# Kernel tuning notes

Measured on AMD Instinct MI355X. Metric: run time of the kernel, lower is better.

Reference implementation:

```python
import jax, jax.numpy as jnp
import numpy as np

N = 20000   # nodes
E = 40000   # directed edges
F_IN = 13   # dataset.num_features
G = 1000    # graphs in batch
DIMS = [(13, 32), (32, 64), (64, 64)]  # (M_in, M_out) per NNConv layer


def setup_inputs() -> dict:
    key = jax.random.key(0)
    ks = list(jax.random.split(key, 32))
    inp = {}
    inp["x"] = jax.random.normal(ks[0], (N, F_IN), jnp.float32)
    inp["edge_index"] = jax.random.randint(ks[1], (2, E), 0, N, dtype=jnp.int32)
    inp["edge_attr"] = jax.random.uniform(ks[2], (E, 5), dtype=jnp.float32)
    inp["batch"] = jnp.sort(jax.random.randint(ks[3], (N,), 0, G, dtype=jnp.int32))
    i = 4
    for l, (mi, mo) in enumerate(DIMS):
        inp[f"w1_{l}"] = jax.random.normal(ks[i], (5, 128), jnp.float32) / np.sqrt(5.0).astype(np.float32); i += 1
        inp[f"b1_{l}"] = jnp.zeros((128,), jnp.float32)
        inp[f"w2_{l}"] = jax.random.normal(ks[i], (128, mi * mo), jnp.float32) / np.sqrt(128.0).astype(np.float32); i += 1
        inp[f"b2_{l}"] = jnp.zeros((mi * mo,), jnp.float32)
        inp[f"root_{l}"] = jax.random.normal(ks[i], (mi, mo), jnp.float32) / np.sqrt(float(mi)).astype(np.float32); i += 1
        inp[f"bias_{l}"] = jnp.zeros((mo,), jnp.float32)
    inp["fc1_w"] = jax.random.normal(ks[i], (64, 32), jnp.float32) / 8.0; i += 1
    inp["fc1_b"] = jnp.zeros((32,), jnp.float32)
    inp["fc2_w"] = jax.random.normal(ks[i], (32, 16), jnp.float32) / np.sqrt(32.0).astype(np.float32); i += 1
    inp["fc2_b"] = jnp.zeros((16,), jnp.float32)
    inp["fc3_w"] = jax.random.normal(ks[i], (16, 1), jnp.float32) / 4.0; i += 1
    inp["fc3_b"] = jnp.zeros((1,), jnp.float32)
    return inp


def _nnconv(x, src, dst, edge_attr, w1, b1, w2, b2, root, bias, mi, mo):
    # edge MLP: [E,5] -> [E,128] -> [E, mi*mo] per-edge weight matrices
    h = jax.nn.relu(edge_attr @ w1 + b1)
    We = (h @ w2 + b2).reshape(-1, mi, mo)          # [E, mi, mo]
    msg = jnp.einsum('ei,eio->eo', x[src], We)      # gather + per-edge matmul
    agg = jax.ops.segment_sum(msg, dst, num_segments=x.shape[0])  # scatter-add
    return x @ root + agg + bias                    # NNConv root weight + bias


def _forward(x, edge_index, edge_attr, batch, convs, fc1_w, fc1_b, fc2_w, fc2_b, fc3_w, fc3_b):
    src, dst = edge_index[0], edge_index[1]
    for (mi, mo), (w1, b1, w2, b2, root, bias) in zip(DIMS, convs):
        x = jax.nn.elu(_nnconv(x, src, dst, edge_attr, w1, b1, w2, b2, root, bias, mi, mo))
    # scatter_mean pooling over graphs
    sums = jax.ops.segment_sum(x, batch, num_segments=G)
    cnt = jax.ops.segment_sum(jnp.ones((x.shape[0],), x.dtype), batch, num_segments=G)
    xg = sums / jnp.maximum(cnt, 1.0)[:, None]
    xg = jax.nn.elu(xg @ fc1_w + fc1_b)
    xg = jax.nn.elu(xg @ fc2_w + fc2_b)
    return (xg @ fc3_w + fc3_b).reshape(-1)


def reference(x, edge_index, edge_attr, batch,
              w1_0, b1_0, w2_0, b2_0, root_0, bias_0,
              w1_1, b1_1, w2_1, b2_1, root_1, bias_1,
              w1_2, b1_2, w2_2, b2_2, root_2, bias_2,
              fc1_w, fc1_b, fc2_w, fc2_b, fc3_w, fc3_b):
    convs = [(w1_0, b1_0, w2_0, b2_0, root_0, bias_0),
             (w1_1, b1_1, w2_1, b2_1, root_1, bias_1),
             (w1_2, b1_2, w2_2, b2_2, root_2, bias_2)]
    return _forward(x, edge_index, edge_attr, batch, convs,
                    fc1_w, fc1_b, fc2_w, fc2_b, fc3_w, fc3_b)
```

## Files before the change

kernel.cpp:

```cpp
#include <hip/hip_runtime.h>
#include <stdint.h>
#include <math.h>

typedef _Float16 half8_t __attribute__((ext_vector_type(8)));
typedef float floatx4 __attribute__((ext_vector_type(4)));

#define NN 20000
#define NE 40000
#define NG 1000
#define NBLK 313
#define NSPLIT 4

__global__ __launch_bounds__(256) void prep_fused_kernel(
    const float* __restrict__ x, _Float16* __restrict__ e16,
    const float* __restrict__ w2a, const float* __restrict__ b2a, _Float16* __restrict__ oa,
    const float* __restrict__ w2b, const float* __restrict__ b2b, _Float16* __restrict__ ob,
    const float* __restrict__ w2c, const float* __restrict__ b2c, _Float16* __restrict__ oc,
    int* __restrict__ deg)
{
  if (blockIdx.x < 1250) {
    int idx = blockIdx.x * 256 + threadIdx.x;
    int n = idx >> 4, i = idx & 15;
    e16[idx] = (i < 13) ? (_Float16)x[(size_t)n * 13 + i] : (_Float16)0.f;
    return;
  }
  if (blockIdx.x >= 1680) {
    int n = (blockIdx.x - 1680) * 256 + threadIdx.x;
    if (n < NN) deg[n] = 0;
    return;
  }
  const int TOT0 = 68 * 2 * 64, TOT1 = 132 * 4 * 64, TOT2 = 264 * 4 * 64;
  int idx = (blockIdx.x - 1250) * 256 + threadIdx.x;
  const float *w2, *b2; _Float16* op; int mi, mo, mpsh, CT;
  if (idx < TOT0) { w2 = w2a; b2 = b2a; op = oa; mi = 13; mo = 32; mpsh = 4; CT = 2; }
  else if (idx < TOT0 + TOT1) { idx -= TOT0; w2 = w2b; b2 = b2b; op = ob; mi = 32; mo = 64; mpsh = 5; CT = 4; }
  else if (idx < TOT0 + TOT1 + TOT2) { idx -= TOT0 + TOT1; w2 = w2c; b2 = b2c; op = oc; mi = 64; mo = 64; mpsh = 6; CT = 4; }
  else return;
  int l = idx & 63;
  int ct = (idx >> 6) % CT;
  int c = idx / (64 * CT);
  int q = l >> 4;
  int n = ct * 16 + (l & 15);
  int mask = (1 << mpsh) - 1;
  half8_t v;
#pragma unroll
  for (int j = 0; j < 8; ++j) {
    int r = c * 32 + q * 8 + j;
    int k = r >> mpsh, i = r & mask;
    float f = 0.f;
    if (i < mi) {
      if (k < 128) f = w2[(size_t)(k * mi + i) * mo + n];
      else if (k == 128) f = b2[(size_t)i * mo + n];
    }
    v[j] = (_Float16)f;
  }
  *(half8_t*)(op + (size_t)idx * 8) = v;
}

__global__ __launch_bounds__(256) void deg_kernel(const int* __restrict__ dst, int* __restrict__ deg) {
  int e = blockIdx.x * 256 + threadIdx.x;
  if (e < NE) atomicAdd(&deg[dst[e]], 1);
}

__global__ __launch_bounds__(1024) void scan_kernel(
    const int* __restrict__ deg, int* __restrict__ row_ptr, int* __restrict__ cursor)
{
  constexpr int CH = 20;
  __shared__ int wsum[16];
  int t = threadIdx.x;
  int lane = t & 63, w = t >> 6;
  int base = t * CH;
  int local[CH];
#pragma unroll
  for (int i = 0; i < CH; ++i) {
    int n = base + i;
    local[i] = (n < NN) ? deg[n] : 0;
  }
  int s = 0;
#pragma unroll
  for (int i = 0; i < CH; ++i) s += local[i];
  int sc = s;
#pragma unroll
  for (int d = 1; d < 64; d <<= 1) {
    int v = __shfl_up(sc, d, 64);
    if (lane >= d) sc += v;
  }
  if (lane == 63) wsum[w] = sc;
  __syncthreads();
  if (w == 0 && lane < 16) {
    int v = wsum[lane];
    int scc = v;
#pragma unroll
    for (int d = 1; d < 16; d <<= 1) {
      int u = __shfl_up(scc, d, 64);
      if (lane >= d) scc += u;
    }
    wsum[lane] = scc - v;
  }
  __syncthreads();
  int run = wsum[w] + (sc - s);
#pragma unroll
  for (int i = 0; i < CH; ++i) {
    int n = base + i;
    if (n < NN) { row_ptr[n] = run; cursor[n] = run; run += local[i]; }
    else if (n == NN) row_ptr[NN] = run;
  }
}

__global__ __launch_bounds__(256) void fill_kernel(
    const int* __restrict__ dst, int* __restrict__ cursor, int* __restrict__ eids)
{
  int e = blockIdx.x * 256 + threadIdx.x;
  if (e < NE) { int p = atomicAdd(&cursor[dst[e]], 1); eids[p] = e; }
}

template <int MIP, int MO, int NCC, int KCNT>
__global__ __launch_bounds__(256, 4) void msg9_kernel(
    const float* __restrict__ ea, const float* __restrict__ w1,
    const float* __restrict__ b1, const _Float16* __restrict__ xe,
    const int* __restrict__ src,
    const _Float16* __restrict__ w2h, _Float16* __restrict__ msgp)
{
  constexpr int CT = MO / 16;
  constexpr int CHB = CT * 1024;
  constexpr int XLSS = MIP + 8;
  constexpr int HSTW = KCNT | 1;
  constexpr int XV = (MIP == 64) ? 2 : 1;
  constexpr int NU2 = MIP / 16;
  constexpr int KH = (KCNT + 1) >> 1;
  constexpr int XB = 128 * XLSS * 2;
  constexpr int HB = 128 * HSTW * 4;
  constexpr int SBYTES = (XB > HB) ? XB : HB;

  __shared__ char sb[SBYTES];
  __shared__ uint4 wsb[2][CHB / 16];
  __shared__ float w1s[5 * 128 + 128];

  _Float16* sxb = (_Float16*)sb;
  unsigned* hls = (unsigned*)sb;

  const int t = threadIdx.x;
  const int wave = t >> 6, lane = t & 63;
  const int l15 = lane & 15, q = lane >> 4;
  const int split = blockIdx.x / NBLK;
  const int e0 = (blockIdx.x % NBLK) * 128;
  const int c0 = NCC * split;
  const int kg0 = KCNT * split;

  {
    int rowA = t >> 1;
    int egA = e0 + rowA; if (egA >= NE) egA = NE - 1;
    const uint4* xr = (const uint4*)(xe + (size_t)src[egA] * MIP);
    uint4* xd = (uint4*)(sxb + rowA * XLSS);
#pragma unroll
    for (int u = 0; u < NU2; ++u) xd[(t & 1) * NU2 + u] = xr[(t & 1) * NU2 + u];
  }
  const int te = t & 127;
  float ear[5];
  {
    int ege = e0 + te; if (ege >= NE) ege = NE - 1;
#pragma unroll
    for (int j = 0; j < 5; ++j) ear[j] = ea[(size_t)ege * 5 + j];
  }
  for (int i = t; i < 768; i += 256) w1s[i] = (i < 640) ? w1[i] : b1[i - 640];
  __syncthreads();

  const int wbase = wave * 32;
  half8_t xf[2][XV];
#pragma unroll
  for (int s = 0; s < 2; ++s) {
    int el = wbase + s * 16 + l15;
    int i0 = (MIP == 16) ? (q & 1) * 8 : q * 8;
    xf[s][0] = *(const half8_t*)(sxb + el * XLSS + i0);
    if constexpr (MIP == 64)
      xf[s][XV - 1] = *(const half8_t*)(sxb + el * XLSS + 32 + q * 8);
  }
  __syncthreads();

  {
    int kh = t >> 7;
    int klo = kh * KH;
    int khi = klo + KH; if (khi > KCNT) khi = KCNT;
    for (int kl = klo; kl < khi; ++kl) {
      int kg = kg0 + kl;
      float v;
      if (kg < 128) {
        v = w1s[640 + kg];
#pragma unroll
        for (int j = 0; j < 5; ++j) v = fmaf(ear[j], w1s[j * 128 + kg], v);
        v = fmaxf(v, 0.f);
      } else v = (kg == 128) ? 1.f : 0.f;
      union { _Float16 f; unsigned short u; } cv; cv.f = (_Float16)v;
      hls[te * HSTW + kl] = (unsigned)cv.u * 0x10001u;
    }
  }
  __syncthreads();

  floatx4 acc[2][CT];
#pragma unroll
  for (int s = 0; s < 2; ++s)
#pragma unroll
    for (int b = 0; b < CT; ++b) acc[s][b] = (floatx4){0.f, 0.f, 0.f, 0.f};

  const char* wgp = (const char*)w2h + (size_t)c0 * CHB;
  uint4 r4; uint2 r2;
  if constexpr (CT == 4) r4 = *(const uint4*)(wgp + t * 16);
  else r2 = *(const uint2*)(wgp + t * 8);

#pragma unroll 2
  for (int cc = 0; cc < NCC; ++cc) {
    if constexpr (CT == 4) wsb[cc & 1][t] = r4;
    else ((uint2*)wsb[cc & 1])[t] = r2;
    __syncthreads();
    if (cc + 1 < NCC) {
      if constexpr (CT == 4) r4 = *(const uint4*)(wgp + (size_t)(cc + 1) * CHB + t * 16);
      else r2 = *(const uint2*)(wgp + (size_t)(cc + 1) * CHB + t * 8);
    }
    const _Float16* wb = (const _Float16*)wsb[cc & 1];
    half8_t bf[CT];
#pragma unroll
    for (int b = 0; b < CT; ++b)
      bf[b] = *(const half8_t*)(wb + (b * 64 + lane) * 8);
    int kl;
    if constexpr (MIP == 64) kl = cc >> 1;
    else if constexpr (MIP == 32) kl = cc;
    else kl = 2 * cc + (q >> 1);
#pragma unroll
    for (int s = 0; s < 2; ++s) {
      _Float16 hv = *(const _Float16*)(hls + (wbase + s * 16 + l15) * HSTW + kl);
      half8_t af;
      if constexpr (MIP == 64) af = xf[s][cc & 1] * hv;
      else af = xf[s][0] * hv;
#pragma unroll
      for (int b = 0; b < CT; ++b)
        acc[s][b] = __builtin_amdgcn_mfma_f32_16x16x32_f16(af, bf[b], acc[s][b], 0, 0, 0);
    }
  }

  _Float16* mp = msgp + (size_t)split * NE * MO;
#pragma unroll
  for (int s = 0; s < 2; ++s) {
    int rowb = wbase + s * 16 + q * 4;
#pragma unroll
    for (int b = 0; b < CT; ++b) {
      int n = b * 16 + l15;
#pragma unroll
      for (int r = 0; r < 4; ++r) {
        int row = rowb + r;
        int e = e0 + row;
        if (e < NE) mp[(size_t)e * MO + n] = (_Float16)acc[s][b][r];
      }
    }
  }
}

template <int MIN_, int XST, int MO, int FINAL>
__global__ __launch_bounds__(256) void gather_kernel(
    const _Float16* __restrict__ e16in, const float* __restrict__ root,
    const float* __restrict__ bias, const int* __restrict__ row_ptr,
    const int* __restrict__ eids, const _Float16* __restrict__ msgp,
    _Float16* __restrict__ oute, float* __restrict__ outf)
{
  constexpr int NPB = 256 / MO;
  int n = blockIdx.x * NPB + threadIdx.x / MO;
  int o = threadIdx.x % MO;
  if (n >= NN) return;
  float a = bias[o];
#pragma unroll
  for (int i = 0; i < MIN_; ++i)
    a = fmaf((float)e16in[(size_t)n * XST + i], root[i * MO + o], a);
  int r0 = row_ptr[n], r1 = row_ptr[n + 1];
  for (int j = r0; j < r1; ++j) {
    int e = eids[j];
#pragma unroll
    for (int s = 0; s < NSPLIT; ++s)
      a += (float)msgp[((size_t)s * NE + e) * MO + o];
  }
  if constexpr (FINAL) {
    outf[(size_t)n * MO + o] = a;
  } else {
    float v = a > 0.f ? a : (expf(a) - 1.f);
    oute[(size_t)n * MO + o] = (_Float16)v;
  }
}

__global__ __launch_bounds__(64) void pool_fc_kernel(
    const float* __restrict__ xn2, const int* __restrict__ batch,
    const float* __restrict__ f1w, const float* __restrict__ f1b,
    const float* __restrict__ f2w, const float* __restrict__ f2b,
    const float* __restrict__ f3w, const float* __restrict__ f3b,
    float* __restrict__ out)
{
  __shared__ float xg[64]; __shared__ float a1[32]; __shared__ float a2[16];
  int g = blockIdx.x, t = threadIdx.x;
  int lo = 0, hi = NN;
  while (lo < hi) { int m = (lo + hi) >> 1; if (batch[m] < g) lo = m + 1; else hi = m; }
  int start = lo; hi = NN;
  while (lo < hi) { int m = (lo + hi) >> 1; if (batch[m] <= g) lo = m + 1; else hi = m; }
  int end = lo;
  float acc = 0.f;
  for (int n = start; n < end; ++n) {
    float v = xn2[(size_t)n * 64 + t];
    acc += v > 0.f ? v : (expf(v) - 1.f);
  }
  float c = (end > start) ? (float)(end - start) : 1.f;
  xg[t] = acc / c;
  __syncthreads();
  if (t < 32) {
    float a = f1b[t];
    for (int i = 0; i < 64; ++i) a = fmaf(xg[i], f1w[i * 32 + t], a);
    a1[t] = a > 0.f ? a : (expf(a) - 1.f);
  }
  __syncthreads();
  if (t < 16) {
    float a = f2b[t];
    for (int i = 0; i < 32; ++i) a = fmaf(a1[i], f2w[i * 16 + t], a);
    a2[t] = a > 0.f ? a : (expf(a) - 1.f);
  }
  __syncthreads();
  if (t == 0) {
    float a = f3b[0];
    for (int i = 0; i < 16; ++i) a = fmaf(a2[i], f3w[i], a);
    out[g] = a;
  }
}

extern "C" void kernel_launch(void* const* d_in, const int* in_sizes, int n_in,
                              void* d_out, int out_size, void* d_ws, size_t ws_size,
                              hipStream_t stream)
{
  const float* x_in  = (const float*)d_in[0];
  const int*   ei    = (const int*)d_in[1];
  const float* ea    = (const float*)d_in[2];
  const int*   batch = (const int*)d_in[3];
  const float* W1[3] = {(const float*)d_in[4],  (const float*)d_in[10], (const float*)d_in[16]};
  const float* B1[3] = {(const float*)d_in[5],  (const float*)d_in[11], (const float*)d_in[17]};
  const float* W2[3] = {(const float*)d_in[6],  (const float*)d_in[12], (const float*)d_in[18]};
  const float* B2[3] = {(const float*)d_in[7],  (const float*)d_in[13], (const float*)d_in[19]};
  const float* RT[3] = {(const float*)d_in[8],  (const float*)d_in[14], (const float*)d_in[20]};
  const float* BS[3] = {(const float*)d_in[9],  (const float*)d_in[15], (const float*)d_in[21]};
  const float* f1w = (const float*)d_in[22]; const float* f1b = (const float*)d_in[23];
  const float* f2w = (const float*)d_in[24]; const float* f2b = (const float*)d_in[25];
  const float* f3w = (const float*)d_in[26]; const float* f3b = (const float*)d_in[27];

  char* ws = (char*)d_ws;
  size_t off = 0;
  auto alloc = [&](size_t bytes) { void* p = ws + off; off += (bytes + 255) & ~(size_t)255; return p; };
  float*    xn2   = (float*)alloc((size_t)NN * 64 * 4);
  _Float16* e16_0 = (_Float16*)alloc((size_t)NN * 16 * 2);
  _Float16* e16_1 = (_Float16*)alloc((size_t)NN * 32 * 2);
  _Float16* e16_2 = (_Float16*)alloc((size_t)NN * 64 * 2);
  _Float16* w2h0  = (_Float16*)alloc((size_t)68 * 2048);
  _Float16* w2h1  = (_Float16*)alloc((size_t)132 * 4096);
  _Float16* w2h2  = (_Float16*)alloc((size_t)264 * 4096);
  _Float16* msgp  = (_Float16*)alloc((size_t)NSPLIT * NE * 64 * 2);
  int*      deg     = (int*)alloc((size_t)NN * 4);
  int*      row_ptr = (int*)alloc((size_t)(NN + 1) * 4);
  int*      cursor  = (int*)alloc((size_t)NN * 4);
  int*      eids    = (int*)alloc((size_t)NE * 4);

  const int* srcp = ei;
  const int* dstp = ei + NE;

  prep_fused_kernel<<<1680 + (NN + 255) / 256, 256, 0, stream>>>(
      x_in, e16_0, W2[0], B2[0], w2h0, W2[1], B2[1], w2h1, W2[2], B2[2], w2h2, deg);
  deg_kernel<<<(NE + 255) / 256, 256, 0, stream>>>(dstp, deg);
  scan_kernel<<<1, 1024, 0, stream>>>(deg, row_ptr, cursor);
  fill_kernel<<<(NE + 255) / 256, 256, 0, stream>>>(dstp, cursor, eids);

  msg9_kernel<16, 32, 17, 34><<<NBLK * NSPLIT, 256, 0, stream>>>(
      ea, W1[0], B1[0], e16_0, srcp, w2h0, msgp);
  gather_kernel<13, 16, 32, 0><<<(NN + 7) / 8, 256, 0, stream>>>(
      e16_0, RT[0], BS[0], row_ptr, eids, msgp, e16_1, xn2);

  msg9_kernel<32, 64, 33, 33><<<NBLK * NSPLIT, 256, 0, stream>>>(
      ea, W1[1], B1[1], e16_1, srcp, w2h1, msgp);
  gather_kernel<32, 32, 64, 0><<<(NN + 3) / 4, 256, 0, stream>>>(
      e16_1, RT[1], BS[1], row_ptr, eids, msgp, e16_2, xn2);

  msg9_kernel<64, 64, 66, 33><<<NBLK * NSPLIT, 256, 0, stream>>>(
      ea, W1[2], B1[2], e16_2, srcp, w2h2, msgp);
  gather_kernel<64, 64, 64, 1><<<(NN + 3) / 4, 256, 0, stream>>>(
      e16_2, RT[2], BS[2], row_ptr, eids, msgp, e16_2, xn2);

  pool_fc_kernel<<<NG, 64, 0, stream>>>(xn2, batch, f1w, f1b, f2w, f2b, f3w, f3b, (float*)d_out);
}
```

Measured before the change: 299.1 us.

## Double edges per block in message kernel to reuse staged W2 chunks

The edge tile per block in the NNConv message kernel grows from 128 to 256 edges. Each wave now computes four 16-edge MFMA row tiles instead of two, so each W2 chunk staged in shared memory is reused across twice as many edges and the grid needs half as many blocks. Each thread now gathers one full source row and computes all hidden activations for one edge, where before two threads shared that work. The cost is more accumulator registers, larger shared memory and lower occupancy (launch bound 3 instead of 4), plus fewer blocks to spread across the CUs.

```diff
diff --git a/kernel.cpp b/kernel.cpp
--- a/kernel.cpp
+++ b/kernel.cpp
@@ -8,7 +8,7 @@
 #define NN 20000
 #define NE 40000
 #define NG 1000
-#define NBLK 313
+#define NBLK 157
 #define NSPLIT 4
 
 __global__ __launch_bounds__(256) void prep_fused_kernel(
@@ -115,21 +115,21 @@
 }
 
 template <int MIP, int MO, int NCC, int KCNT>
-__global__ __launch_bounds__(256, 4) void msg9_kernel(
+__global__ __launch_bounds__(256, 3) void msg9_kernel(
     const float* __restrict__ ea, const float* __restrict__ w1,
     const float* __restrict__ b1, const _Float16* __restrict__ xe,
     const int* __restrict__ src,
     const _Float16* __restrict__ w2h, _Float16* __restrict__ msgp)
 {
+  constexpr int EPB = 256;
   constexpr int CT = MO / 16;
   constexpr int CHB = CT * 1024;
   constexpr int XLSS = MIP + 8;
   constexpr int HSTW = KCNT | 1;
   constexpr int XV = (MIP == 64) ? 2 : 1;
-  constexpr int NU2 = MIP / 16;
-  constexpr int KH = (KCNT + 1) >> 1;
-  constexpr int XB = 128 * XLSS * 2;
-  constexpr int HB = 128 * HSTW * 4;
+  constexpr int NU4 = MIP / 8;
+  constexpr int XB = EPB * XLSS * 2;
+  constexpr int HB = EPB * HSTW * 4;
   constexpr int SBYTES = (XB > HB) ? XB : HB;
 
   __shared__ char sb[SBYTES];
@@ -143,32 +143,30 @@
   const int wave = t >> 6, lane = t & 63;
   const int l15 = lane & 15, q = lane >> 4;
   const int split = blockIdx.x / NBLK;
-  const int e0 = (blockIdx.x % NBLK) * 128;
+  const int e0 = (blockIdx.x % NBLK) * EPB;
   const int c0 = NCC * split;
   const int kg0 = KCNT * split;
 
   {
-    int rowA = t >> 1;
-    int egA = e0 + rowA; if (egA >= NE) egA = NE - 1;
-    const uint4* xr = (const uint4*)(xe + (size_t)src[egA] * MIP);
-    uint4* xd = (uint4*)(sxb + rowA * XLSS);
-#pragma unroll
-    for (int u = 0; u < NU2; ++u) xd[(t & 1) * NU2 + u] = xr[(t & 1) * NU2 + u];
-  }
-  const int te = t & 127;
+    int eg = e0 + t; if (eg >= NE) eg = NE - 1;
+    const uint4* xr = (const uint4*)(xe + (size_t)src[eg] * MIP);
+    uint4* xd = (uint4*)(sxb + t * XLSS);
+#pragma unroll
+    for (int u = 0; u < NU4; ++u) xd[u] = xr[u];
+  }
   float ear[5];
   {
-    int ege = e0 + te; if (ege >= NE) ege = NE - 1;
-#pragma unroll
-    for (int j = 0; j < 5; ++j) ear[j] = ea[(size_t)ege * 5 + j];
+    int eg = e0 + t; if (eg >= NE) eg = NE - 1;
+#pragma unroll
+    for (int j = 0; j < 5; ++j) ear[j] = ea[(size_t)eg * 5 + j];
   }
   for (int i = t; i < 768; i += 256) w1s[i] = (i < 640) ? w1[i] : b1[i - 640];
   __syncthreads();
 
-  const int wbase = wave * 32;
-  half8_t xf[2][XV];
-#pragma unroll
-  for (int s = 0; s < 2; ++s) {
+  const int wbase = wave * 64;
+  half8_t xf[4][XV];
+#pragma unroll
+  for (int s = 0; s < 4; ++s) {
     int el = wbase + s * 16 + l15;
     int i0 = (MIP == 16) ? (q & 1) * 8 : q * 8;
     xf[s][0] = *(const half8_t*)(sxb + el * XLSS + i0);
@@ -177,28 +175,23 @@
   }
   __syncthreads();
 
-  {
-    int kh = t >> 7;
-    int klo = kh * KH;
-    int khi = klo + KH; if (khi > KCNT) khi = KCNT;
-    for (int kl = klo; kl < khi; ++kl) {
-      int kg = kg0 + kl;
-      float v;
-      if (kg < 128) {
-        v = w1s[640 + kg];
-#pragma unroll
-        for (int j = 0; j < 5; ++j) v = fmaf(ear[j], w1s[j * 128 + kg], v);
-        v = fmaxf(v, 0.f);
-      } else v = (kg == 128) ? 1.f : 0.f;
-      union { _Float16 f; unsigned short u; } cv; cv.f = (_Float16)v;
-      hls[te * HSTW + kl] = (unsigned)cv.u * 0x10001u;
-    }
-  }
-  __syncthreads();
-
-  floatx4 acc[2][CT];
-#pragma unroll
-  for (int s = 0; s < 2; ++s)
+  for (int kl = 0; kl < KCNT; ++kl) {
+    int kg = kg0 + kl;
+    float v;
+    if (kg < 128) {
+      v = w1s[640 + kg];
+#pragma unroll
+      for (int j = 0; j < 5; ++j) v = fmaf(ear[j], w1s[j * 128 + kg], v);
+      v = fmaxf(v, 0.f);
+    } else v = (kg == 128) ? 1.f : 0.f;
+    union { _Float16 f; unsigned short u; } cv; cv.f = (_Float16)v;
+    hls[t * HSTW + kl] = (unsigned)cv.u * 0x10001u;
+  }
+  __syncthreads();
+
+  floatx4 acc[4][CT];
+#pragma unroll
+  for (int s = 0; s < 4; ++s)
 #pragma unroll
     for (int b = 0; b < CT; ++b) acc[s][b] = (floatx4){0.f, 0.f, 0.f, 0.f};
 
@@ -226,7 +219,7 @@
     else if constexpr (MIP == 32) kl = cc;
     else kl = 2 * cc + (q >> 1);
 #pragma unroll
-    for (int s = 0; s < 2; ++s) {
+    for (int s = 0; s < 4; ++s) {
       _Float16 hv = *(const _Float16*)(hls + (wbase + s * 16 + l15) * HSTW + kl);
       half8_t af;
       if constexpr (MIP == 64) af = xf[s][cc & 1] * hv;
@@ -239,7 +232,7 @@
 
   _Float16* mp = msgp + (size_t)split * NE * MO;
 #pragma unroll
-  for (int s = 0; s < 2; ++s) {
+  for (int s = 0; s < 4; ++s) {
     int rowb = wbase + s * 16 + q * 4;
 #pragma unroll
     for (int b = 0; b < CT; ++b) {
```

Result: no change. 302.6 us (+1.2%).
